# Kernel tuning notes

Hardware: AMD Instinct MI355X
Metric: run time of the kernel (lower is better)

The kernel has to match this reference:

```python
import jax, jax.numpy as jnp
import numpy as np

N_CLASSES = 512


def setup_inputs() -> dict:
    key = jax.random.key(0)
    k1, k2 = jax.random.split(key)
    B, T, C, V = 16, 2048, 1, 256
    x0 = jax.random.normal(k1, (B, T, C, V), dtype=jnp.float32)
    # nn.Parameter(torch.randn(...) * embedding_scale) with embedding_scale = 0.001
    embedding0 = jax.random.normal(k2, (C, N_CLASSES, V), dtype=jnp.float32) * 0.001
    return {"x0": x0, "embedding0": embedding0}


def reference(x0, embedding0):
    # normalize=False path: x = x0, embedding = embedding0
    B, T, C, V = x0.shape
    K = embedding0.shape[1]
    x = x0
    emb = embedding0

    # Nearest-codebook search. Original materializes (chunk, C, K, V) diffs and
    # (same argmin) to avoid the huge broadcasted intermediate.
    x1 = x.reshape(B * T, C, V)                      # (N, C, V)
    x_sq = jnp.sum(x1 * x1, axis=-1)[:, :, None]     # (N, C, 1)
    e_sq = jnp.sum(emb * emb, axis=-1)[None]         # (1, C, K)
    cross = jnp.einsum('ncv,ckv->nck', x1, emb)      # (N, C, K)
    d2 = x_sq - 2.0 * cross + e_sq                   # (N, C, K)
    index = jnp.argmin(d2, axis=2)                   # (N, C) int

    # entropy of code usage (histogram over all selected indices)
    hist = jnp.bincount(index.reshape(-1), length=K).astype(jnp.float32)
    prob = hist / jnp.float32(index.shape[0])        # divide by N = len(index)
    entropy = -jnp.sum(jnp.where(hist > 0, prob * jnp.log(prob), 0.0))

    # gather codebook vectors
    offset = jnp.arange(C, dtype=index.dtype) * K    # (C,)
    index1 = (index + offset[None, :]).reshape(-1)   # (N*C,)
    output = emb.reshape(C * K, V)[index1].reshape(B, T, C, V)

    # straight-through output + VQ / commitment losses
    out0 = jax.lax.stop_gradient(output - x) + x
    out1 = jnp.sum((jax.lax.stop_gradient(x) - output) ** 2, axis=3)   # (B,T,C)
    out2 = jnp.sum((x - jax.lax.stop_gradient(output)) ** 2, axis=3) \
         + jnp.sum((x - x0) ** 2, axis=3)                              # zero term when normalize=False
    return out0, out1, out2, entropy
```

## Files before the change

### kernel.cpp

```cpp
#include <hip/hip_runtime.h>
#include <math.h>

#define NV 256
#define NK 512
#define TSH 4096
#define SLABR 128

typedef unsigned short u16;
typedef unsigned int u32;
using short8  = __attribute__((ext_vector_type(8))) short;
using floatx4 = __attribute__((ext_vector_type(4))) float;

__device__ __forceinline__ u16 f2bf(float f) {
    unsigned int u = __float_as_uint(f);
    u += 0x7fffu + ((u >> 16) & 1u);
    return (u16)(u >> 16);
}
__device__ __forceinline__ floatx4 mfma16(short8 a, short8 b, floatx4 c) {
    return __builtin_amdgcn_mfma_f32_16x16x32_bf16(a, b, c, 0, 0, 0);
}

__global__ __launch_bounds__(256) void vq_prepcvt(const float* __restrict__ emb,
                                                  float* __restrict__ esq1,
                                                  u16* __restrict__ ehws,
                                                  int* __restrict__ hist) {
    const int t = threadIdx.x;
    const int lane = t & 63;
    const int code = blockIdx.x * 4 + (t >> 6);
    const int nt = code >> 4, c = code & 15;
    const float4 v = *(const float4*)(emb + (size_t)code * NV + lane * 4);
    ushort4 h;
    h.x = f2bf(v.x);
    h.y = f2bf(v.y);
    h.z = f2bf(v.z);
    h.w = f2bf(v.w);
    const size_t base = (size_t)nt * TSH + (size_t)(lane >> 1) * 128 + c * 8 + (lane & 1) * 4;
    *(ushort4*)(ehws + base) = h;
    float s = v.x * v.x + v.y * v.y + v.z * v.z + v.w * v.w;
#pragma unroll
    for (int m = 1; m <= 32; m <<= 1) s += __shfl_xor(s, m, 64);
    if (lane == 0) esq1[code] = s + 2.0f;
    const int g = blockIdx.x * 256 + t;
    if (g < NK) hist[g] = 0;
}

__global__ __launch_bounds__(1024, 4) void vq_main(
    const float* __restrict__ x,
    const float* __restrict__ emb,
    const u16* __restrict__ ehws,
    const float* __restrict__ esq1,
    int* __restrict__ hist,
    float* __restrict__ out0,
    float* __restrict__ out1,
    float* __restrict__ out2) {
    __shared__ u16 xl[2][16 * NV];
    __shared__ u32 kall[8][16][16];
    __shared__ u32 idx_lds[SLABR];

    const int t = threadIdx.x;
    const int wid = t >> 6;
    const int lane = t & 63;
    const int lr = lane & 15;
    const int lg = lane >> 4;
    const size_t row0 = (size_t)blockIdx.x * SLABR;

    const u16* bb0 = ehws + (size_t)(2 * wid) * TSH + lane * 8;
    const u16* bb1 = ehws + (size_t)(2 * wid + 1) * TSH + lane * 8;
    short8 b0[8], b1[8];
#pragma unroll
    for (int ks = 0; ks < 8; ++ks) {
        b0[ks] = *(const short8*)(bb0 + ks * 512);
        b1[ks] = *(const short8*)(bb1 + ks * 512);
    }
    const int cbase0 = (2 * wid) * 16 + lg * 4;
    const int cbase1 = (2 * wid + 1) * 16 + lg * 4;
    float evq0[4], evq1[4];
#pragma unroll
    for (int j = 0; j < 4; ++j) {
        evq0[j] = esq1[cbase0 + j];
        evq1[j] = esq1[cbase1 + j];
    }

#define XLOAD(XR, TAU)                                                         \
    XR = *(const float4*)(x + (row0 + (TAU) * 16 + wid) * NV + lane * 4)
#define XWRITE(XR, BUF) do {                                                   \
        u32 lo = (u32)f2bf(XR.x) | ((u32)f2bf(XR.y) << 16);                    \
        u32 hi = (u32)f2bf(XR.z) | ((u32)f2bf(XR.w) << 16);                    \
        int byte = wid * 512 + ((lane * 8) ^ ((wid & 7) << 4));                \
        *(uint2*)((char*)&xl[BUF][0] + byte) = make_uint2(lo, hi);             \
    } while (0)

    float4 xr;
    XLOAD(xr, 0);
    XWRITE(xr, 0);
    __syncthreads();

    u32 rmin_tau[8];

#pragma unroll
    for (int tau = 0; tau < 8; ++tau) {
        const int buf = tau & 1;
        if (tau < 7) XLOAD(xr, tau + 1);

        floatx4 a0e = {0.f,0.f,0.f,0.f}, a0o = {0.f,0.f,0.f,0.f};
        floatx4 a1e = {0.f,0.f,0.f,0.f}, a1o = {0.f,0.f,0.f,0.f};
#pragma unroll
        for (int ks = 0; ks < 8; ++ks) {
            int byte = lr * 512 + ((ks * 64 + lg * 16) ^ ((lr & 7) << 4));
            short8 a = *(const short8*)((const char*)&xl[buf][0] + byte);
            if (ks & 1) { a0o = mfma16(b0[ks], a, a0o); a1o = mfma16(b1[ks], a, a1o); }
            else        { a0e = mfma16(b0[ks], a, a0e); a1e = mfma16(b1[ks], a, a1e); }
        }
        u32 k = 0xffffffffu;
#pragma unroll
        for (int j = 0; j < 4; ++j) {
            float d0 = fmaf(-2.0f, a0e[j] + a0o[j], evq0[j]);
            float d1 = fmaf(-2.0f, a1e[j] + a1o[j], evq1[j]);
            u32 k0 = (__float_as_uint(d0) & 0xfffffe00u) | (u32)(cbase0 + j);
            u32 k1 = (__float_as_uint(d1) & 0xfffffe00u) | (u32)(cbase1 + j);
            k = min(k, min(k0, k1));
        }
        rmin_tau[tau] = k;

        if (tau < 7) XWRITE(xr, buf ^ 1);
        __syncthreads();
    }
#undef XLOAD
#undef XWRITE

#pragma unroll
    for (int tau = 0; tau < 8; ++tau) {
        u32 k = rmin_tau[tau];
        k = min(k, (u32)__shfl_xor((int)k, 16, 64));
        k = min(k, (u32)__shfl_xor((int)k, 32, 64));
        if (lane < 16) kall[tau][wid][lane] = k;
    }
    __syncthreads();

    if (t < SLABR) {
        u32 v = 0xffffffffu;
#pragma unroll
        for (int w = 0; w < 16; ++w) v = min(v, kall[t >> 4][w][t & 15]);
        const int idx = (int)(v & 511u);
        idx_lds[t] = (u32)idx;
        atomicAdd(&hist[idx], 1);
    }
    __syncthreads();

    const size_t rb = row0 + (size_t)wid * 8;
#pragma unroll
    for (int batch = 0; batch < 2; ++batch) {
        const int r0 = batch * 4;
        int idx4[4];
#pragma unroll
        for (int rr = 0; rr < 4; ++rr) idx4[rr] = (int)idx_lds[wid * 8 + r0 + rr];
        float4 xv[4], ev[4];
#pragma unroll
        for (int rr = 0; rr < 4; ++rr) {
            const size_t row = rb + r0 + rr;
            xv[rr] = *(const float4*)(x + row * NV + lane * 4);
            ev[rr] = *(const float4*)(emb + (size_t)idx4[rr] * NV + lane * 4);
        }
        float s[4];
#pragma unroll
        for (int rr = 0; rr < 4; ++rr) {
            const size_t row = rb + r0 + rr;
            float4 o;
            o.x = (ev[rr].x - xv[rr].x) + xv[rr].x;
            o.y = (ev[rr].y - xv[rr].y) + xv[rr].y;
            o.z = (ev[rr].z - xv[rr].z) + xv[rr].z;
            o.w = (ev[rr].w - xv[rr].w) + xv[rr].w;
            *(float4*)(out0 + row * NV + lane * 4) = o;
            float d0 = xv[rr].x - ev[rr].x, d1 = xv[rr].y - ev[rr].y;
            float d2 = xv[rr].z - ev[rr].z, d3 = xv[rr].w - ev[rr].w;
            s[rr] = d0 * d0 + d1 * d1 + d2 * d2 + d3 * d3;
        }
#pragma unroll
        for (int rr = 0; rr < 4; ++rr) {
#pragma unroll
            for (int m = 1; m <= 32; m <<= 1) s[rr] += __shfl_xor(s[rr], m, 64);
        }
        if (lane == 0) {
#pragma unroll
            for (int rr = 0; rr < 4; ++rr) {
                out1[rb + r0 + rr] = s[rr];
                out2[rb + r0 + rr] = s[rr];
            }
        }
    }
}

__global__ __launch_bounds__(256) void vq_entropy(const int* __restrict__ hist,
                                                  float* __restrict__ out_ent,
                                                  int n_rows) {
    __shared__ float sdata[256];
    int t = threadIdx.x;
    float local = 0.0f;
    float invn = 1.0f / (float)n_rows;
    for (int k = t; k < NK; k += 256) {
        int h = hist[k];
        if (h > 0) {
            float p = (float)h * invn;
            local += p * logf(p);
        }
    }
    sdata[t] = local;
    __syncthreads();
    for (int s = 128; s >= 1; s >>= 1) {
        if (t < s) sdata[t] += sdata[t + s];
        __syncthreads();
    }
    if (t == 0) *out_ent = -sdata[0];
}

extern "C" void kernel_launch(void* const* d_in, const int* in_sizes, int n_in,
                              void* d_out, int out_size, void* d_ws, size_t ws_size,
                              hipStream_t stream) {
    const float* x   = (const float*)d_in[0];
    const float* emb = (const float*)d_in[1];

    const int n_rows = in_sizes[0] / NV;

    float* out0 = (float*)d_out;
    float* out1 = out0 + (size_t)n_rows * NV;
    float* out2 = out1 + n_rows;
    float* ent  = out2 + n_rows;

    float* esq1  = (float*)d_ws;
    int* hist    = (int*)(esq1 + NK);
    u16* ehws    = (u16*)(hist + NK + 4);

    vq_prepcvt<<<NK / 4, 256, 0, stream>>>(emb, esq1, ehws, hist);
    vq_main<<<n_rows / SLABR, 1024, 0, stream>>>(x, emb, ehws, esq1, hist,
                                                 out0, out1, out2);
    vq_entropy<<<1, 256, 0, stream>>>(hist, ent, n_rows);
}
```

Measured before the change: 46.05 us.

## Stage whole 128-row x slab in LDS upfront, drop per-step barriers

Loads all eight 16-row x tiles into registers at kernel start, converts them to bf16 and writes them into a single 64KB LDS slab, then runs the eight MFMA distance steps without any intermediate __syncthreads. This removes the double-buffered load/convert/barrier pipeline and its seven block-wide barriers, and issues all global loads at once for more memory-level parallelism. In exchange it raises LDS use from 16KB to 64KB per block and adds 32 registers of float4 staging, which can lower occupancy, and the compute cannot start until the whole slab has arrived.

Result: slower. 57.14 us (+24.1%).

```diff
diff --git a/kernel.cpp b/kernel.cpp
--- a/kernel.cpp
+++ b/kernel.cpp
@@ -53,7 +53,7 @@
     float* __restrict__ out0,
     float* __restrict__ out1,
     float* __restrict__ out2) {
-    __shared__ u16 xl[2][16 * NV];
+    __shared__ u16 xl[8 * 16 * NV];
     __shared__ u32 kall[8][16][16];
     __shared__ u32 idx_lds[SLABR];
 
@@ -64,6 +64,11 @@
     const int lg = lane >> 4;
     const size_t row0 = (size_t)blockIdx.x * SLABR;
 
+    float4 xr[8];
+#pragma unroll
+    for (int tau = 0; tau < 8; ++tau)
+        xr[tau] = *(const float4*)(x + (row0 + tau * 16 + wid) * NV + lane * 4);
+
     const u16* bb0 = ehws + (size_t)(2 * wid) * TSH + lane * 8;
     const u16* bb1 = ehws + (size_t)(2 * wid + 1) * TSH + lane * 8;
     short8 b0[8], b1[8];
@@ -81,33 +86,24 @@
         evq1[j] = esq1[cbase1 + j];
     }
 
-#define XLOAD(XR, TAU)                                                         \
-    XR = *(const float4*)(x + (row0 + (TAU) * 16 + wid) * NV + lane * 4)
-#define XWRITE(XR, BUF) do {                                                   \
-        u32 lo = (u32)f2bf(XR.x) | ((u32)f2bf(XR.y) << 16);                    \
-        u32 hi = (u32)f2bf(XR.z) | ((u32)f2bf(XR.w) << 16);                    \
-        int byte = wid * 512 + ((lane * 8) ^ ((wid & 7) << 4));                \
-        *(uint2*)((char*)&xl[BUF][0] + byte) = make_uint2(lo, hi);             \
-    } while (0)
-
-    float4 xr;
-    XLOAD(xr, 0);
-    XWRITE(xr, 0);
+#pragma unroll
+    for (int tau = 0; tau < 8; ++tau) {
+        u32 lo = (u32)f2bf(xr[tau].x) | ((u32)f2bf(xr[tau].y) << 16);
+        u32 hi = (u32)f2bf(xr[tau].z) | ((u32)f2bf(xr[tau].w) << 16);
+        int byte = tau * 8192 + wid * 512 + ((lane * 8) ^ ((wid & 7) << 4));
+        *(uint2*)((char*)xl + byte) = make_uint2(lo, hi);
+    }
     __syncthreads();
 
     u32 rmin_tau[8];
-
 #pragma unroll
     for (int tau = 0; tau < 8; ++tau) {
-        const int buf = tau & 1;
-        if (tau < 7) XLOAD(xr, tau + 1);
-
         floatx4 a0e = {0.f,0.f,0.f,0.f}, a0o = {0.f,0.f,0.f,0.f};
         floatx4 a1e = {0.f,0.f,0.f,0.f}, a1o = {0.f,0.f,0.f,0.f};
 #pragma unroll
         for (int ks = 0; ks < 8; ++ks) {
-            int byte = lr * 512 + ((ks * 64 + lg * 16) ^ ((lr & 7) << 4));
-            short8 a = *(const short8*)((const char*)&xl[buf][0] + byte);
+            int byte = tau * 8192 + lr * 512 + ((ks * 64 + lg * 16) ^ ((lr & 7) << 4));
+            short8 a = *(const short8*)((const char*)xl + byte);
             if (ks & 1) { a0o = mfma16(b0[ks], a, a0o); a1o = mfma16(b1[ks], a, a1o); }
             else        { a0e = mfma16(b0[ks], a, a0e); a1e = mfma16(b1[ks], a, a1e); }
         }
@@ -121,12 +117,7 @@
             k = min(k, min(k0, k1));
         }
         rmin_tau[tau] = k;
-
-        if (tau < 7) XWRITE(xr, buf ^ 1);
-        __syncthreads();
-    }
-#undef XLOAD
-#undef XWRITE
+    }
 
 #pragma unroll
     for (int tau = 0; tau < 8; ++tau) {
```
